# Kernel tuning notes

Measured on AMD Instinct MI355X. Metric: run time of the kernel, lower is better.

The kernel has to match this reference:

```python
import jax, jax.numpy as jnp
import numpy as np

DIM = 512
HEADS = 8
DH = DIM // HEADS          # 64, dim_head = dim // 8
M = DIM // 2               # 256 landmarks
ITERS = 6                  # pinv iterations
KS = 33                    # residual depthwise conv kernel (lucidrains default)
N_LAYERS = 2
LN_EPS = 1e-5


def layer_norm(x, scale, bias):
    mu = x.mean(-1, keepdims=True)
    var = ((x - mu) ** 2).mean(-1, keepdims=True)
    return (x - mu) * jax.lax.rsqrt(var + LN_EPS) * scale + bias


def sinusoidal_pe(T, d, dtype):
    pos = np.arange(T)[:, None]
    div = np.exp(np.arange(0, d, 2) * (-np.log(10000.0) / d))
    pe = np.zeros((T, d), dtype=np.float32)
    pe[:, 0::2] = np.sin(pos * div)
    pe[:, 1::2] = np.cos(pos * div)
    return jnp.asarray(pe, dtype=dtype)


def iter_pinv(x):
    # Newton-Schulz Moore-Penrose iteration (lucidrains), global-max scaling
    ax = jnp.abs(x)
    denom = ax.sum(-1).max() * ax.sum(-2).max()
    z = jnp.swapaxes(x, -1, -2) / denom
    I = jnp.eye(x.shape[-1], dtype=x.dtype)
    for _ in range(ITERS):
        xz = x @ z
        z = 0.25 * (z @ (13.0 * I - xz @ (15.0 * I - xz @ (7.0 * I - xz))))
    return z


def nystrom_attention(x, qkv_w, out_w, out_b, conv_w):
    b, n, d = x.shape
    pad = (-n) % M                       # left-pad so seq divisible by M
    xp = jnp.pad(x, ((0, 0), (pad, 0), (0, 0)))
    N = n + pad
    q, k, v = [t.reshape(b, N, HEADS, DH).transpose(0, 2, 1, 3)
               for t in jnp.split(xp @ qkv_w, 3, axis=-1)]  # each [b,h,N,dh]
    q = q * (DH ** -0.5)
    l = N // M                           # segment length per landmark
    q_l = q.reshape(b, HEADS, M, l, DH).mean(3)   # [b,h,M,dh]
    k_l = k.reshape(b, HEADS, M, l, DH).mean(3)
    attn1 = jax.nn.softmax(jnp.einsum('bhid,bhjd->bhij', q, k_l), -1)    # [b,h,N,M]
    attn2 = jax.nn.softmax(jnp.einsum('bhid,bhjd->bhij', q_l, k_l), -1)  # [b,h,M,M]
    attn3 = jax.nn.softmax(jnp.einsum('bhid,bhjd->bhij', q_l, k), -1)    # [b,h,M,N]
    out = attn1 @ (iter_pinv(attn2) @ (attn3 @ v))                       # [b,h,N,dh]
    # residual depthwise conv over sequence, per head (groups=heads)
    P = KS // 2
    out = out + jax.lax.conv_general_dilated(
        v, conv_w, (1, 1), ((P, P), (0, 0)),
        dimension_numbers=('NCHW', 'OIHW', 'NCHW'), feature_group_count=HEADS)
    out = out.transpose(0, 2, 1, 3).reshape(b, N, d)
    out = out @ out_w + out_b
    return out[:, -n:]


def setup_inputs() -> dict:
    key = jax.random.key(0)
    ks = jax.random.split(key, 12)
    B, T, IN_DIM = 4, 4095, 1024
    s = 0.02
    return {
        'data': jax.random.normal(ks[0], (B, T, IN_DIM), jnp.float32),
        'fc1_w': jax.random.normal(ks[1], (IN_DIM, DIM), jnp.float32) * s,
        'fc1_b': jnp.zeros((DIM,), jnp.float32),
        'cls_token': jax.random.normal(ks[2], (1, 1, DIM), jnp.float32),
        'ln_scale': jnp.ones((N_LAYERS, DIM), jnp.float32),
        'ln_bias': jnp.zeros((N_LAYERS, DIM), jnp.float32),
        'qkv_w': jax.random.normal(ks[3], (N_LAYERS, DIM, 3 * DIM), jnp.float32) * s,
        'out_w': jax.random.normal(ks[4], (N_LAYERS, DIM, DIM), jnp.float32) * s,
        'out_b': jnp.zeros((N_LAYERS, DIM), jnp.float32),
        'conv_w': jax.random.normal(ks[5], (N_LAYERS, HEADS, 1, KS, 1), jnp.float32) * s,
        'fnorm_scale': jnp.ones((DIM,), jnp.float32),
        'fnorm_bias': jnp.zeros((DIM,), jnp.float32),
        'fcout_w': jax.random.normal(ks[6], (DIM, 1), jnp.float32) * s,
        'fcout_b': jnp.zeros((1,), jnp.float32),
    }


def reference(data, fc1_w, fc1_b, cls_token, ln_scale, ln_bias, qkv_w, out_w,
              out_b, conv_w, fnorm_scale, fnorm_bias, fcout_w, fcout_b):
    B, T, _ = data.shape
    h = jax.nn.relu(data @ fc1_w + fc1_b)
    h = h + sinusoidal_pe(T, DIM, h.dtype)
    cls = jnp.broadcast_to(cls_token, (B, 1, DIM))
    h = jnp.concatenate([cls, h], axis=1)
    for i in range(N_LAYERS):
        h = h + nystrom_attention(layer_norm(h, ln_scale[i], ln_bias[i]),
                                  qkv_w[i], out_w[i], out_b[i], conv_w[i])
    h = layer_norm(h, fnorm_scale, fnorm_bias)
    logits = (h[:, 0] @ fcout_w + fcout_b)[:, 0]
    y_prob = jax.nn.sigmoid(logits)
    y_hat = (y_prob > 0.5).astype(jnp.int32)
    return logits, y_prob, y_hat
```

## Files before the change

### kernel.cpp

```cpp
#include <hip/hip_runtime.h>
#include <math.h>

typedef long long ll;
typedef __attribute__((ext_vector_type(8))) short short8;
typedef __attribute__((ext_vector_type(4))) float f32x4;

#define NBATCH 4
#define TSEQ   4095
#define NTOK   4096
#define DMODEL 512
#define NHEAD  8
#define DHEAD  64
#define NLAND  256
#define INDIM  1024
#define KCONV  33
#define NBH    32
#define NSPLIT 8

__device__ __forceinline__ float bred(float* red, float v, int tid, int op){
  red[tid] = v; __syncthreads();
  for (int s = 128; s > 0; s >>= 1){
    if (tid < s) red[tid] = op ? fmaxf(red[tid], red[tid+s]) : (red[tid] + red[tid+s]);
    __syncthreads();
  }
  float r = red[0];
  __syncthreads();
  return r;
}

__device__ __forceinline__ short f2bf(float f){
  unsigned u = __float_as_uint(f);
  u += 0x7fff + ((u>>16)&1);
  return (short)(u>>16);
}
__device__ __forceinline__ float bf2f(short s){
  return __uint_as_float(((unsigned)(unsigned short)s) << 16);
}

__global__ __launch_bounds__(256) void pe_table_k(float* __restrict__ pe){
  int idx = blockIdx.x*256 + threadIdx.x;
  if (idx >= TSEQ*DMODEL) return;
  int c = idx & 511; int t = idx >> 9;
  const double NEG = -9.210340371976184 / 512.0;
  double div = exp((double)(c & ~1) * NEG);
  double ang = (double)t * div;
  pe[idx] = (c & 1) ? (float)cos(ang) : (float)sin(ang);
}

__global__ __launch_bounds__(256) void pe_cls_add_k(float* __restrict__ hb, const float* __restrict__ cls,
                                                    const float* __restrict__ pe){
  ll idx = (ll)blockIdx.x*256 + threadIdx.x;
  int c = (int)(idx & 511);
  ll rn = idx >> 9;
  int n = (int)(rn & 4095);
  if (n == 0) hb[idx] = cls[c];
  else        hb[idx] += pe[(ll)(n-1)*512 + c];
}

__global__ __launch_bounds__(256) void ln_rows_k(const float* __restrict__ in, short* __restrict__ out,
                                                 const float* __restrict__ sc, const float* __restrict__ bi){
  __shared__ float red[256];
  ll row = blockIdx.x;
  const float* xr = in + row*DMODEL;
  short* orow = out + row*DMODEL;
  int tid = threadIdx.x;
  float v0 = xr[tid], v1 = xr[tid+256];
  float mu = bred(red, v0+v1, tid, 0) * (1.f/512.f);
  float d0 = v0-mu, d1 = v1-mu;
  float var = bred(red, d0*d0 + d1*d1, tid, 0) * (1.f/512.f);
  float inv = 1.f / sqrtf(var + 1e-5f);
  orow[tid]     = f2bf(d0*inv*sc[tid]     + bi[tid]);
  orow[tid+256] = f2bf(d1*inv*sc[tid+256] + bi[tid+256]);
}

template<int BM, int BN, int AB, int BB, int CB, int SW>
__global__ __launch_bounds__(256)
void mgemm(const void* __restrict__ Av, const void* __restrict__ Bv,
           void* __restrict__ Cv, const void* __restrict__ Ev,
           const float* __restrict__ bias,
           int Mr, int K, int lda, int ldb, int ldc,
           ll sA, ll sB, ll sC,
           float c0, float c1, int flags)
{
  constexpr int MI = BM/32, NJ = BN/32;
  __shared__ __align__(16) short As[BM*64];
  __shared__ __align__(16) short Bs[BN*64];
  int z = blockIdx.z;
  int bx = blockIdx.x, by = blockIdx.y;
  if (SW){
    int nwg = gridDim.x*gridDim.y;
    int lin = by*gridDim.x + bx;
    int q = nwg >> 3, r = nwg & 7;
    int xcd = lin & 7, idx = lin >> 3;
    int wg = (xcd < r) ? (xcd*(q+1) + idx) : (r*(q+1) + (xcd - r)*q + idx);
    bx = wg % gridDim.x; by = wg / gridDim.x;
  }
  int n0 = bx*BN, m0 = by*BM;
  int tid = threadIdx.x;
  int lane = tid & 63, w = tid >> 6;
  int wr = w >> 1, wc = w & 1;
  int l15 = lane & 15, l4 = lane >> 4;

  f32x4 acc[MI][NJ];
  #pragma unroll
  for (int i = 0; i < MI; i++)
    #pragma unroll
    for (int j = 0; j < NJ; j++) acc[i][j] = (f32x4){0.f,0.f,0.f,0.f};

  for (int k0 = 0; k0 < K; k0 += 64){
    #pragma unroll
    for (int it = 0; it < BM/32; ++it){
      int tau = tid + 256*it;
      int row = tau >> 3, slot = tau & 7;
      int grow = m0 + row;
      short8 v;
      if (AB){
        if (grow < Mr) v = *(const short8*)((const short*)Av + (ll)z*sA + (ll)grow*lda + k0 + slot*8);
        else v = (short8){0,0,0,0,0,0,0,0};
      } else {
        f32x4 p0 = {0.f,0.f,0.f,0.f}, p1 = {0.f,0.f,0.f,0.f};
        if (grow < Mr){
          const float* ap = (const float*)Av + (ll)z*sA + (ll)grow*lda + k0 + slot*8;
          p0 = *(const f32x4*)ap; p1 = *(const f32x4*)(ap+4);
        }
        v[0]=f2bf(p0[0]); v[1]=f2bf(p0[1]); v[2]=f2bf(p0[2]); v[3]=f2bf(p0[3]);
        v[4]=f2bf(p1[0]); v[5]=f2bf(p1[1]); v[6]=f2bf(p1[2]); v[7]=f2bf(p1[3]);
      }
      ((short8*)As)[row*8 + (slot ^ (row&7))] = v;
    }
    #pragma unroll
    for (int it = 0; it < BN/32; ++it){
      int tau = tid + 256*it;
      int n = tau & (BN-1), slot = tau >> (BN==128 ? 7 : 6);
      short8 v;
      if (BB){
        const short* bp = (const short*)Bv + (ll)z*sB + (ll)(k0 + slot*8)*ldb + n0 + n;
        #pragma unroll
        for (int i = 0; i < 8; i++) v[i] = bp[(ll)i*ldb];
      } else {
        const float* bp = (const float*)Bv + (ll)z*sB + (ll)(k0 + slot*8)*ldb + n0 + n;
        #pragma unroll
        for (int i = 0; i < 8; i++) v[i] = f2bf(bp[(ll)i*ldb]);
      }
      ((short8*)Bs)[n*8 + (slot ^ (n&7))] = v;
    }
    __syncthreads();
    #pragma unroll
    for (int kc = 0; kc < 2; kc++){
      short8 af[MI], bfr[NJ];
      #pragma unroll
      for (int i = 0; i < MI; i++){
        int row = wr*(BM/2) + i*16 + l15;
        int g = kc*4 + l4;
        af[i] = ((short8*)As)[row*8 + (g ^ (row&7))];
      }
      #pragma unroll
      for (int j = 0; j < NJ; j++){
        int col = wc*(BN/2) + j*16 + l15;
        int g = kc*4 + l4;
        bfr[j] = ((short8*)Bs)[col*8 + (g ^ (col&7))];
      }
      #pragma unroll
      for (int i = 0; i < MI; i++)
        #pragma unroll
        for (int j = 0; j < NJ; j++)
          acc[i][j] = __builtin_amdgcn_mfma_f32_16x16x32_bf16(af[i], bfr[j], acc[i][j], 0, 0, 0);
    }
    __syncthreads();
  }

  #pragma unroll
  for (int i = 0; i < MI; i++){
    int rbase = m0 + wr*(BM/2) + i*16 + l4*4;
    #pragma unroll
    for (int j = 0; j < NJ; j++){
      int col = n0 + wc*(BN/2) + j*16 + l15;
      #pragma unroll
      for (int r = 0; r < 4; r++){
        int m = rbase + r;
        if (m >= Mr) continue;
        float v = acc[i][j][r];
        if (flags & 4){
          float ev = CB ? bf2f(((const short*)Ev + (ll)z*sC)[(ll)m*ldc + col])
                        : ((const float*)Ev + (ll)z*sC)[(ll)m*ldc + col];
          v = c0 * ev + c1 * v;
        }
        if (flags & 1) v += bias[col];
        if (flags & 2) v = fmaxf(v, 0.f);
        int om = (flags & 16) ? (m + m/TSEQ + 1) : m;
        ll ci = (ll)z*sC + (ll)om*ldc + col;
        if (CB){
          short* Cs = (short*)Cv;
          if (flags & 8) v += bf2f(Cs[ci]);
          Cs[ci] = f2bf(v);
        } else {
          float* Cf = (float*)Cv;
          if (flags & 8) v += Cf[ci];
          Cf[ci] = v;
        }
      }
    }
  }
}

__global__ __launch_bounds__(256)
void gemm_nt(const short* __restrict__ A, const short* __restrict__ Bm, float* __restrict__ C,
             int lda, int ldb, int ldc,
             ll sAb, ll sAh, ll sBb, ll sBh, ll sCb, ll sCh,
             float alpha)
{
  __shared__ float As[64][65];
  __shared__ float Bs[64][65];
  int z = blockIdx.z; int b = z >> 3; int h = z & 7;
  A  += (ll)b*sAb + (ll)h*sAh;
  Bm += (ll)b*sBb + (ll)h*sBh;
  C  += (ll)b*sCb + (ll)h*sCh;
  int n0 = blockIdx.x*64, m0 = blockIdx.y*64;
  int tid = threadIdx.x;
  int kk = tid & 63, rr = tid >> 6;
  #pragma unroll
  for (int r = 0; r < 16; r++){
    As[rr + 4*r][kk] = bf2f(A [(ll)(m0 + rr + 4*r)*lda + kk]);
    Bs[rr + 4*r][kk] = bf2f(Bm[(ll)(n0 + rr + 4*r)*ldb + kk]);
  }
  __syncthreads();
  int tx = tid & 15, ty = tid >> 4;
  float acc[4][4] = {};
  for (int k = 0; k < 64; k++){
    float a[4], bv[4];
    #pragma unroll
    for (int i = 0; i < 4; i++) a[i] = As[ty + 16*i][k];
    #pragma unroll
    for (int j = 0; j < 4; j++) bv[j] = Bs[tx + 16*j][k];
    #pragma unroll
    for (int i = 0; i < 4; i++)
      #pragma unroll
      for (int j = 0; j < 4; j++)
        acc[i][j] += a[i]*bv[j];
  }
  #pragma unroll
  for (int i = 0; i < 4; i++)
    #pragma unroll
    for (int j = 0; j < 4; j++)
      C[(ll)(m0 + ty + 16*i)*ldc + n0 + tx + 16*j] = alpha * acc[i][j];
}

__global__ __launch_bounds__(256)
void mflash_k(const short* __restrict__ Q, const short* __restrict__ K,
              const short* __restrict__ V, short* __restrict__ O,
              int ldq, int ldk, int ldv, int ldo, int nkeys, float alpha,
              ll sQb, ll sQh, ll sKb, ll sKh, ll sVb, ll sVh, ll sOb, ll sOh)
{
  __shared__ __align__(16) short Qs[64*64];
  __shared__ __align__(16) short Ks[64*64];
  __shared__ __align__(16) short Vs[64*64];
  __shared__ __align__(16) short Ps[64*64];
  __shared__ float Sl[64][68];
  __shared__ float m_l[64], s_l[64], scl[64];
  int z = blockIdx.z; int b = z >> 3; int h = z & 7;
  Q += (ll)b*sQb + (ll)h*sQh;
  K += (ll)b*sKb + (ll)h*sKh;
  V += (ll)b*sVb + (ll)h*sVh;
  O += (ll)b*sOb + (ll)h*sOh;
  int m0 = blockIdx.x*64;
  int tid = threadIdx.x;
  int lane = tid & 63, w = tid >> 6;
  int l15 = lane & 15, l4 = lane >> 4;
  int wr = w >> 1, wc = w & 1;

  #pragma unroll
  for (int it = 0; it < 2; it++){
    int tau = tid + 256*it;
    int row = tau >> 3, slot = tau & 7;
    short8 v = *(const short8*)(Q + (ll)(m0 + row)*ldq + slot*8);
    ((short8*)Qs)[row*8 + (slot ^ (row&7))] = v;
  }
  if (tid < 64){ m_l[tid] = -1e30f; s_l[tid] = 0.f; }
  f32x4 o[2][2];
  #pragma unroll
  for (int i = 0; i < 2; i++)
    #pragma unroll
    for (int j = 0; j < 2; j++) o[i][j] = (f32x4){0.f,0.f,0.f,0.f};

  for (int n0 = 0; n0 < nkeys; n0 += 64){
    __syncthreads();
    #pragma unroll
    for (int it = 0; it < 2; it++){
      int tau = tid + 256*it;
      int row = tau >> 3, slot = tau & 7;
      short8 v = *(const short8*)(K + (ll)(n0 + row)*ldk + slot*8);
      ((short8*)Ks)[row*8 + (slot ^ (row&7))] = v;
    }
    #pragma unroll
    for (int it = 0; it < 2; it++){
      int key = (tid >> 3) + 32*it;
      int d0 = (tid & 7)*8;
      short8 v = *(const short8*)(V + (ll)(n0 + key)*ldv + d0);
      #pragma unroll
      for (int j = 0; j < 8; j++){
        int d = d0 + j;
        Vs[d*64 + (((key>>3) ^ (d&7))<<3) + (key&7)] = v[j];
      }
    }
    __syncthreads();
    f32x4 s[2][2];
    #pragma unroll
    for (int i = 0; i < 2; i++)
      #pragma unroll
      for (int j = 0; j < 2; j++) s[i][j] = (f32x4){0.f,0.f,0.f,0.f};
    #pragma unroll
    for (int kc = 0; kc < 2; kc++){
      short8 aq[2], bk[2];
      int g = kc*4 + l4;
      #pragma unroll
      for (int i = 0; i < 2; i++){
        int row = wr*32 + i*16 + l15;
        aq[i] = ((short8*)Qs)[row*8 + (g ^ (row&7))];
      }
      #pragma unroll
      for (int j = 0; j < 2; j++){
        int key = wc*32 + j*16 + l15;
        bk[j] = ((short8*)Ks)[key*8 + (g ^ (key&7))];
      }
      #pragma unroll
      for (int i = 0; i < 2; i++)
        #pragma unroll
        for (int j = 0; j < 2; j++)
          s[i][j] = __builtin_amdgcn_mfma_f32_16x16x32_bf16(aq[i], bk[j], s[i][j], 0, 0, 0);
    }
    #pragma unroll
    for (int i = 0; i < 2; i++)
      #pragma unroll
      for (int j = 0; j < 2; j++)
        #pragma unroll
        for (int r = 0; r < 4; r++)
          Sl[wr*32 + i*16 + l4*4 + r][wc*32 + j*16 + l15] = s[i][j][r] * alpha;
    __syncthreads();
    {
      int row = tid >> 2, q = tid & 3, cb = q*16;
      float sv[16];
      float cmax = -1e30f;
      #pragma unroll
      for (int cc = 0; cc < 16; cc++){ sv[cc] = Sl[row][cb+cc]; cmax = fmaxf(cmax, sv[cc]); }
      cmax = fmaxf(cmax, __shfl_xor(cmax, 1));
      cmax = fmaxf(cmax, __shfl_xor(cmax, 2));
      float mprev = m_l[row];
      float newm = fmaxf(mprev, cmax);
      float lsum = 0.f;
      short8 pv0, pv1;
      #pragma unroll
      for (int cc = 0; cc < 8; cc++){ float e = expf(sv[cc]-newm); lsum += e; pv0[cc] = f2bf(e); }
      #pragma unroll
      for (int cc = 0; cc < 8; cc++){ float e = expf(sv[8+cc]-newm); lsum += e; pv1[cc] = f2bf(e); }
      lsum += __shfl_xor(lsum, 1);
      lsum += __shfl_xor(lsum, 2);
      ((short8*)Ps)[row*8 + ((2*q)   ^ (row&7))] = pv0;
      ((short8*)Ps)[row*8 + ((2*q+1) ^ (row&7))] = pv1;
      if (q == 0){
        float scale = expf(mprev - newm);
        m_l[row] = newm;
        s_l[row] = s_l[row]*scale + lsum;
        scl[row] = scale;
      }
    }
    __syncthreads();
    #pragma unroll
    for (int i = 0; i < 2; i++)
      #pragma unroll
      for (int r = 0; r < 4; r++){
        float sc = scl[wr*32 + i*16 + l4*4 + r];
        #pragma unroll
        for (int j = 0; j < 2; j++) o[i][j][r] *= sc;
      }
    #pragma unroll
    for (int kc = 0; kc < 2; kc++){
      short8 ap[2], bv[2];
      int g = kc*4 + l4;
      #pragma unroll
      for (int i = 0; i < 2; i++){
        int row = wr*32 + i*16 + l15;
        ap[i] = ((short8*)Ps)[row*8 + (g ^ (row&7))];
      }
      #pragma unroll
      for (int j = 0; j < 2; j++){
        int d = wc*32 + j*16 + l15;
        bv[j] = ((short8*)Vs)[d*8 + (g ^ (d&7))];
      }
      #pragma unroll
      for (int i = 0; i < 2; i++)
        #pragma unroll
        for (int j = 0; j < 2; j++)
          o[i][j] = __builtin_amdgcn_mfma_f32_16x16x32_bf16(ap[i], bv[j], o[i][j], 0, 0, 0);
    }
  }
  #pragma unroll
  for (int i = 0; i < 2; i++)
    #pragma unroll
    for (int j = 0; j < 2; j++)
      #pragma unroll
      for (int r = 0; r < 4; r++){
        int row = wr*32 + i*16 + l4*4 + r;
        int col = wc*32 + j*16 + l15;
        O[(ll)(m0 + row)*ldo + col] = f2bf(o[i][j][r] / s_l[row]);
      }
}

__global__ __launch_bounds__(256)
void mflash3_part_k(const short* __restrict__ Q, const short* __restrict__ K,
                    const short* __restrict__ V,
                    float* __restrict__ po, float* __restrict__ pm, float* __restrict__ pl,
                    int ldq, int ldk, int ldv,
                    ll sQb, ll sQh, ll sKb, ll sKh, ll sVb, ll sVh)
{
  __shared__ __align__(16) short Qs[64*64];
  __shared__ __align__(16) short Ks[64*64];
  __shared__ __align__(16) short Vs[64*64];
  __shared__ __align__(16) short Ps[64*64];
  __shared__ float Sl[64][68];
  __shared__ float m_l[64], s_l[64], scl[64];
  int z = blockIdx.z; int b = z >> 3; int h = z & 7;
  int split = blockIdx.y;
  Q += (ll)b*sQb + (ll)h*sQh;
  K += (ll)b*sKb + (ll)h*sKh;
  V += (ll)b*sVb + (ll)h*sVh;
  int m0 = blockIdx.x*64;
  int koff = split * (NTOK/NSPLIT);
  int tid = threadIdx.x;
  int lane = tid & 63, w = tid >> 6;
  int l15 = lane & 15, l4 = lane >> 4;
  int wr = w >> 1, wc = w & 1;

  #pragma unroll
  for (int it = 0; it < 2; it++){
    int tau = tid + 256*it;
    int row = tau >> 3, slot = tau & 7;
    short8 v = *(const short8*)(Q + (ll)(m0 + row)*ldq + slot*8);
    ((short8*)Qs)[row*8 + (slot ^ (row&7))] = v;
  }
  if (tid < 64){ m_l[tid] = -1e30f; s_l[tid] = 0.f; }
  f32x4 o[2][2];
  #pragma unroll
  for (int i = 0; i < 2; i++)
    #pragma unroll
    for (int j = 0; j < 2; j++) o[i][j] = (f32x4){0.f,0.f,0.f,0.f};

  for (int n0 = koff; n0 < koff + NTOK/NSPLIT; n0 += 64){
    __syncthreads();
    #pragma unroll
    for (int it = 0; it < 2; it++){
      int tau = tid + 256*it;
      int row = tau >> 3, slot = tau & 7;
      short8 v = *(const short8*)(K + (ll)(n0 + row)*ldk + slot*8);
      ((short8*)Ks)[row*8 + (slot ^ (row&7))] = v;
    }
    #pragma unroll
    for (int it = 0; it < 2; it++){
      int key = (tid >> 3) + 32*it;
      int d0 = (tid & 7)*8;
      short8 v = *(const short8*)(V + (ll)(n0 + key)*ldv + d0);
      #pragma unroll
      for (int j = 0; j < 8; j++){
        int d = d0 + j;
        Vs[d*64 + (((key>>3) ^ (d&7))<<3) + (key&7)] = v[j];
      }
    }
    __syncthreads();
    f32x4 s[2][2];
    #pragma unroll
    for (int i = 0; i < 2; i++)
      #pragma unroll
      for (int j = 0; j < 2; j++) s[i][j] = (f32x4){0.f,0.f,0.f,0.f};
    #pragma unroll
    for (int kc = 0; kc < 2; kc++){
      short8 aq[2], bk[2];
      int g = kc*4 + l4;
      #pragma unroll
      for (int i = 0; i < 2; i++){
        int row = wr*32 + i*16 + l15;
        aq[i] = ((short8*)Qs)[row*8 + (g ^ (row&7))];
      }
      #pragma unroll
      for (int j = 0; j < 2; j++){
        int key = wc*32 + j*16 + l15;
        bk[j] = ((short8*)Ks)[key*8 + (g ^ (key&7))];
      }
      #pragma unroll
      for (int i = 0; i < 2; i++)
        #pragma unroll
        for (int j = 0; j < 2; j++)
          s[i][j] = __builtin_amdgcn_mfma_f32_16x16x32_bf16(aq[i], bk[j], s[i][j], 0, 0, 0);
    }
    #pragma unroll
    for (int i = 0; i < 2; i++)
      #pragma unroll
      for (int j = 0; j < 2; j++)
        #pragma unroll
        for (int r = 0; r < 4; r++)
          Sl[wr*32 + i*16 + l4*4 + r][wc*32 + j*16 + l15] = s[i][j][r];
    __syncthreads();
    {
      int row = tid >> 2, q = tid & 3, cb = q*16;
      float sv[16];
      float cmax = -1e30f;
      #pragma unroll
      for (int cc = 0; cc < 16; cc++){ sv[cc] = Sl[row][cb+cc]; cmax = fmaxf(cmax, sv[cc]); }
      cmax = fmaxf(cmax, __shfl_xor(cmax, 1));
      cmax = fmaxf(cmax, __shfl_xor(cmax, 2));
      float mprev = m_l[row];
      float newm = fmaxf(mprev, cmax);
      float lsum = 0.f;
      short8 pv0, pv1;
      #pragma unroll
      for (int cc = 0; cc < 8; cc++){ float e = expf(sv[cc]-newm); lsum += e; pv0[cc] = f2bf(e); }
      #pragma unroll
      for (int cc = 0; cc < 8; cc++){ float e = expf(sv[8+cc]-newm); lsum += e; pv1[cc] = f2bf(e); }
      lsum += __shfl_xor(lsum, 1);
      lsum += __shfl_xor(lsum, 2);
      ((short8*)Ps)[row*8 + ((2*q)   ^ (row&7))] = pv0;
      ((short8*)Ps)[row*8 + ((2*q+1) ^ (row&7))] = pv1;
      if (q == 0){
        float scale = expf(mprev - newm);
        m_l[row] = newm;
        s_l[row] = s_l[row]*scale + lsum;
        scl[row] = scale;
      }
    }
    __syncthreads();
    #pragma unroll
    for (int i = 0; i < 2; i++)
      #pragma unroll
      for (int r = 0; r < 4; r++){
        float sc = scl[wr*32 + i*16 + l4*4 + r];
        #pragma unroll
        for (int j = 0; j < 2; j++) o[i][j][r] *= sc;
      }
    #pragma unroll
    for (int kc = 0; kc < 2; kc++){
      short8 ap[2], bv[2];
      int g = kc*4 + l4;
      #pragma unroll
      for (int i = 0; i < 2; i++){
        int row = wr*32 + i*16 + l15;
        ap[i] = ((short8*)Ps)[row*8 + (g ^ (row&7))];
      }
      #pragma unroll
      for (int j = 0; j < 2; j++){
        int d = wc*32 + j*16 + l15;
        bv[j] = ((short8*)Vs)[d*8 + (g ^ (d&7))];
      }
      #pragma unroll
      for (int i = 0; i < 2; i++)
        #pragma unroll
        for (int j = 0; j < 2; j++)
          o[i][j] = __builtin_amdgcn_mfma_f32_16x16x32_bf16(ap[i], bv[j], o[i][j], 0, 0, 0);
    }
  }
  int bs = z*NSPLIT + split;
  #pragma unroll
  for (int i = 0; i < 2; i++)
    #pragma unroll
    for (int j = 0; j < 2; j++)
      #pragma unroll
      for (int r = 0; r < 4; r++){
        int row = wr*32 + i*16 + l4*4 + r;
        int col = wc*32 + j*16 + l15;
        po[((ll)bs*NLAND + m0 + row)*64 + col] = o[i][j][r];
      }
  if (tid < 64){
    pm[(ll)bs*NLAND + m0 + tid] = m_l[tid];
    pl[(ll)bs*NLAND + m0 + tid] = s_l[tid];
  }
}

__global__ __launch_bounds__(256)
void flash3_comb_k(const float* __restrict__ po, const float* __restrict__ pm,
                   const float* __restrict__ pl, short* __restrict__ av){
  int bh = blockIdx.y;
  int row = blockIdx.x*4 + (threadIdx.x >> 6);
  int col = threadIdx.x & 63;
  float ms = -1e30f;
  float mv[NSPLIT];
  #pragma unroll
  for (int s = 0; s < NSPLIT; s++){
    mv[s] = pm[((ll)bh*NSPLIT + s)*NLAND + row];
    ms = fmaxf(ms, mv[s]);
  }
  float osum = 0.f, lsum = 0.f;
  #pragma unroll
  for (int s = 0; s < NSPLIT; s++){
    float wgt = expf(mv[s] - ms);
    osum += wgt * po[(((ll)bh*NSPLIT + s)*NLAND + row)*64 + col];
    lsum += wgt * pl[((ll)bh*NSPLIT + s)*NLAND + row];
  }
  av[((ll)bh*NLAND + row)*64 + col] = f2bf(osum / lsum);
}

__global__ __launch_bounds__(256) void softmax_rows_k(float* __restrict__ data, short* __restrict__ out16,
                                                      int cols){
  __shared__ float red[256];
  float* row = data + (ll)blockIdx.x * cols;
  short* row16 = out16 ? out16 + (ll)blockIdx.x * cols : nullptr;
  int tid = threadIdx.x;
  float m = -1e30f;
  for (int c = tid; c < cols; c += 256) m = fmaxf(m, row[c]);
  m = bred(red, m, tid, 1);
  float s = 0.f;
  for (int c = tid; c < cols; c += 256){ float e = expf(row[c] - m); row[c] = e; s += e; }
  s = bred(red, s, tid, 0);
  float inv = 1.f/s;
  for (int c = tid; c < cols; c += 256){
    float p = row[c] * inv;
    row[c] = p;
    if (row16) row16[c] = f2bf(p);
  }
}

__global__ __launch_bounds__(256) void landmarks_k(const short* __restrict__ qkv,
                                                   short* __restrict__ ql, short* __restrict__ kl){
  int idx = blockIdx.x*256 + threadIdx.x;
  int d = idx & 63;
  int i = (idx >> 6) & 255;
  int h = (idx >> 14) & 7;
  int b = idx >> 17;
  const short* base = qkv + ((ll)b*NTOK + (ll)i*16)*1536 + h*64 + d;
  float sq = 0.f, sk = 0.f;
  #pragma unroll
  for (int l = 0; l < 16; l++){ sq += bf2f(base[l*1536]); sk += bf2f(base[l*1536 + 512]); }
  ql[idx] = f2bf(sq * (0.125f/16.f));
  kl[idx] = f2bf(sk * (1.f/16.f));
}

__global__ void init_scal_k(unsigned* s){ s[0] = 0u; s[1] = 0u; }

__global__ __launch_bounds__(256) void a2_maxsums_k(const float* __restrict__ a2, unsigned* __restrict__ gm){
  __shared__ float red[256];
  const float* A = a2 + (ll)blockIdx.x*65536;
  int tid = threadIdx.x;
  float cs = 0.f, rs = 0.f;
  for (int i = 0; i < 256; i++) cs += A[i*256 + tid];
  for (int j = 0; j < 256; j++) rs += A[tid*256 + j];
  float cmax = bred(red, cs, tid, 1);
  float rmax = bred(red, rs, tid, 1);
  if (tid == 0){
    atomicMax(gm + 0, __float_as_uint(rmax));
    atomicMax(gm + 1, __float_as_uint(cmax));
  }
}

__global__ __launch_bounds__(256) void zinit_k(const float* __restrict__ a2, short* __restrict__ z,
                                               const unsigned* __restrict__ gm){
  float inv = 1.f / (__uint_as_float(gm[0]) * __uint_as_float(gm[1]));
  int idx = blockIdx.x*256 + threadIdx.x;
  int j = idx & 255, i = (idx >> 8) & 255, bh = idx >> 16;
  z[idx] = f2bf(a2[(ll)bh*65536 + j*256 + i] * inv);
}

__global__ __launch_bounds__(256) void dwconv_add_k(const short* __restrict__ qkv,
                                                    const float* __restrict__ cw, short* __restrict__ out){
  __shared__ float sv[160][64];
  __shared__ float w[KCONV];
  int z = blockIdx.y; int b = z >> 3; int h = z & 7;
  int t0 = blockIdx.x * 128;
  int tid = threadIdx.x;
  if (tid < KCONV) w[tid] = cw[h*KCONV + tid];
  const short* vbase = qkv + (ll)b*NTOK*1536 + 1024 + h*64;
  for (int e = tid; e < 160*64; e += 256){
    int r = e >> 6, d = e & 63;
    int t = t0 - 16 + r;
    sv[r][d] = (t >= 0 && t < NTOK) ? bf2f(vbase[(ll)t*1536 + d]) : 0.f;
  }
  __syncthreads();
  short* obase = out + (ll)b*NTOK*512 + h*64;
  for (int e = tid; e < 128*64; e += 256){
    int r = e >> 6, d = e & 63;
    float s = 0.f;
    #pragma unroll
    for (int kk = 0; kk < KCONV; kk++) s += sv[r+kk][d]*w[kk];
    ll oi = (ll)(t0+r)*512 + d;
    obase[oi] = f2bf(bf2f(obase[oi]) + s);
  }
}

__global__ __launch_bounds__(256) void head_k(const float* __restrict__ hb, const float* __restrict__ fns,
      const float* __restrict__ fnb, const float* __restrict__ fw, const float* __restrict__ fb,
      float* __restrict__ out){
  __shared__ float red[256];
  int b = blockIdx.x;
  const float* xr = hb + (ll)b*NTOK*DMODEL;
  int tid = threadIdx.x;
  float v0 = xr[tid], v1 = xr[tid+256];
  float mu = bred(red, v0+v1, tid, 0) * (1.f/512.f);
  float d0 = v0-mu, d1 = v1-mu;
  float var = bred(red, d0*d0 + d1*d1, tid, 0) * (1.f/512.f);
  float inv = 1.f/sqrtf(var + 1e-5f);
  float y0 = d0*inv*fns[tid]     + fnb[tid];
  float y1 = d1*inv*fns[tid+256] + fnb[tid+256];
  float dot = bred(red, y0*fw[tid] + y1*fw[tid+256], tid, 0);
  if (tid == 0){
    float logit = dot + fb[0];
    float prob = 1.f/(1.f + expf(-logit));
    out[b] = logit; out[4+b] = prob; out[8+b] = (prob > 0.5f) ? 1.f : 0.f;
  }
}

extern "C" void kernel_launch(void* const* d_in, const int* in_sizes, int n_in,
                              void* d_out, int out_size, void* d_ws, size_t ws_size,
                              hipStream_t stream)
{
  (void)in_sizes; (void)n_in; (void)out_size;
  const float* data  = (const float*)d_in[0];
  const float* fc1_w = (const float*)d_in[1];
  const float* fc1_b = (const float*)d_in[2];
  const float* cls   = (const float*)d_in[3];
  const float* ln_s  = (const float*)d_in[4];
  const float* ln_b  = (const float*)d_in[5];
  const float* qkv_w = (const float*)d_in[6];
  const float* out_w = (const float*)d_in[7];
  const float* out_b = (const float*)d_in[8];
  const float* convw = (const float*)d_in[9];
  const float* fns   = (const float*)d_in[10];
  const float* fnb   = (const float*)d_in[11];
  const float* fcw   = (const float*)d_in[12];
  const float* fcb   = (const float*)d_in[13];
  float* out = (float*)d_out;
  float* ws  = (float*)d_ws;

  float* h    = ws;
  short* xb   = (short*)(h + 8388608);
  short* qkvh = xb + 8388608;
  short* ql   = qkvh + 25165824;
  short* kl   = ql + 524288;
  float* a2f  = (float*)(kl + 524288);
  short* a2h  = (short*)(a2f + 2097152);
  short* zA   = a2h + 2097152;
  short* zB   = zA + 2097152;
  short* t1   = zB + 2097152;
  short* t2   = t1 + 2097152;
  short* t3   = t2 + 2097152;
  short* av   = t3 + 2097152;
  short* y2   = av + 524288;
  float* po   = (float*)(y2 + 524288);
  float* pm   = po + 4194304;
  float* pl   = pm + 65536;
  float* pe   = pl + 65536;
  unsigned* scal = (unsigned*)(pe + 2097152);

  const size_t NEED = (size_t)((char*)(scal + 2) - (char*)ws);
  if (ws_size < NEED) return;

  pe_table_k<<<(TSEQ*DMODEL + 255)/256, 256, 0, stream>>>(pe);
  mgemm<128,128,0,0,0,1><<<dim3(4, 128, 1), 256, 0, stream>>>(
      data, fc1_w, h, nullptr, fc1_b,
      NBATCH*TSEQ, INDIM, INDIM, DMODEL, DMODEL,
      0, 0, 0, 0.f, 0.f, 1|2|16);
  pe_cls_add_k<<<(NBATCH*NTOK*DMODEL)/256, 256, 0, stream>>>(h, cls, pe);

  for (int L = 0; L < 2; L++){
    const float* qw = qkv_w + (ll)L*DMODEL*1536;
    const float* ow = out_w + (ll)L*DMODEL*DMODEL;
    const float* ob = out_b + (ll)L*DMODEL;
    const float* cw = convw + (ll)L*NHEAD*KCONV;

    ln_rows_k<<<NBATCH*NTOK, 256, 0, stream>>>(h, xb, ln_s + L*DMODEL, ln_b + L*DMODEL);
    mgemm<128,128,1,0,1,1><<<dim3(12, 128, 1), 256, 0, stream>>>(
        xb, qw, qkvh, nullptr, nullptr,
        NBATCH*NTOK, DMODEL, DMODEL, 1536, 1536,
        0, 0, 0, 0.f, 0.f, 0);
    landmarks_k<<<2048, 256, 0, stream>>>(qkvh, ql, kl);

    gemm_nt<<<dim3(4, 4, NBH), 256, 0, stream>>>(
        ql, kl, a2f, 64, 64, 256,
        131072, 16384, 131072, 16384, 524288, 65536, 1.f);
    softmax_rows_k<<<NBH*NLAND, 256, 0, stream>>>(a2f, a2h, 256);

    init_scal_k<<<1, 1, 0, stream>>>(scal);
    a2_maxsums_k<<<NBH, 256, 0, stream>>>(a2f, scal);
    zinit_k<<<8192, 256, 0, stream>>>(a2f, zA, scal);

    short* zc = zA; short* zn = zB;
    for (int it = 0; it < 6; it++){
      mgemm<64,64,1,1,1,0><<<dim3(4, 4, NBH), 256, 0, stream>>>(
          a2h, zc, t1, nullptr, nullptr, 256, 256, 256, 256, 256,
          65536, 65536, 65536, 0.f, 0.f, 0);
      mgemm<64,64,1,1,1,0><<<dim3(4, 4, NBH), 256, 0, stream>>>(
          t1, t1, t2, t1, nullptr, 256, 256, 256, 256, 256,
          65536, 65536, 65536, 7.f, -1.f, 4);
      mgemm<64,64,1,1,1,0><<<dim3(4, 4, NBH), 256, 0, stream>>>(
          t1, t2, t3, t1, nullptr, 256, 256, 256, 256, 256,
          65536, 65536, 65536, 15.f, -1.f, 4);
      mgemm<64,64,1,1,1,0><<<dim3(4, 4, NBH), 256, 0, stream>>>(
          zc, t3, zn, zc, nullptr, 256, 256, 256, 256, 256,
          65536, 65536, 65536, 3.25f, -0.25f, 4);
      short* tmp = zc; zc = zn; zn = tmp;
    }

    mflash3_part_k<<<dim3(4, NSPLIT, NBH), 256, 0, stream>>>(
        ql, qkvh + 512, qkvh + 1024, po, pm, pl,
        64, 1536, 1536,
        131072, 16384, (ll)NTOK*1536, 64, (ll)NTOK*1536, 64);
    flash3_comb_k<<<dim3(64, NBH), 256, 0, stream>>>(po, pm, pl, av);

    mgemm<64,64,1,1,1,0><<<dim3(1, 4, NBH), 256, 0, stream>>>(
        zc, av, y2, nullptr, nullptr, 256, 256, 256, 64, 64,
        65536, 16384, 16384, 0.f, 0.f, 0);

    mflash_k<<<dim3(64, 1, NBH), 256, 0, stream>>>(
        qkvh, kl, y2, xb,
        1536, 64, 64, 512, NLAND, 0.125f,
        (ll)NTOK*1536, 64, 131072, 16384, 131072, 16384, (ll)NTOK*512, 64);

    dwconv_add_k<<<dim3(32, NBH), 256, 0, stream>>>(qkvh, cw, xb);

    mgemm<128,128,1,0,0,1><<<dim3(4, 128, 1), 256, 0, stream>>>(
        xb, ow, h, nullptr, ob,
        NBATCH*NTOK, DMODEL, DMODEL, DMODEL, DMODEL,
        0, 0, 0, 0.f, 0.f, 1|8);
  }

  head_k<<<4, 256, 0, stream>>>(h, fns, fnb, fcw, fcb, out);
}
```

Before: 1.300 ms.

## Pre-convert inputs and weights to bf16 with transposed weight layout for GEMMs

Adds kernels that convert the input data to bf16 and transpose the fc1, qkv and out weight matrices into an N-major bf16 layout. A new B-load mode lets the big GEMMs read B with contiguous 16-byte vector loads instead of eight strided scalar fp32 loads with in-loop conversion. The positional-encoding table now uses float sin/cos instead of double precision. This costs extra workspace and a few extra launches plus one pass over the input data, and the float trig may change PE values slightly at large positions.

Result: no change. 1.308 ms (+0.6%).

```diff
diff --git a/kernel.cpp b/kernel.cpp
--- a/kernel.cpp
+++ b/kernel.cpp
@@ -43,8 +43,8 @@
   int c = idx & 511; int t = idx >> 9;
   const double NEG = -9.210340371976184 / 512.0;
   double div = exp((double)(c & ~1) * NEG);
-  double ang = (double)t * div;
-  pe[idx] = (c & 1) ? (float)cos(ang) : (float)sin(ang);
+  float ang = (float)((double)t * div);
+  pe[idx] = (c & 1) ? cosf(ang) : sinf(ang);
 }
 
 __global__ __launch_bounds__(256) void pe_cls_add_k(float* __restrict__ hb, const float* __restrict__ cls,
@@ -57,6 +57,37 @@
   else        hb[idx] += pe[(ll)(n-1)*512 + c];
 }
 
+__global__ __launch_bounds__(256) void cvt_bf16_k(const float* __restrict__ in, short* __restrict__ out, int n8){
+  int idx = blockIdx.x*256 + threadIdx.x;
+  for (int i = idx; i < n8; i += gridDim.x*256){
+    const f32x4* p = (const f32x4*)(in + (ll)i*8);
+    f32x4 a = p[0], b = p[1];
+    short8 v;
+    v[0]=f2bf(a[0]); v[1]=f2bf(a[1]); v[2]=f2bf(a[2]); v[3]=f2bf(a[3]);
+    v[4]=f2bf(b[0]); v[5]=f2bf(b[1]); v[6]=f2bf(b[2]); v[7]=f2bf(b[3]);
+    ((short8*)out)[i] = v;
+  }
+}
+
+__global__ __launch_bounds__(256) void transpose_bf16_k(const float* __restrict__ in, short* __restrict__ out,
+                                                        int K, int N, ll sIn, ll sOut){
+  __shared__ float t[64][65];
+  int L = blockIdx.z;
+  in  += (ll)L*sIn;
+  out += (ll)L*sOut;
+  int n0 = blockIdx.x*64, k0 = blockIdx.y*64;
+  int tid = threadIdx.x;
+  for (int e = tid; e < 4096; e += 256){
+    int r = e >> 6, c = e & 63;
+    t[r][c] = in[(ll)(k0 + r)*N + n0 + c];
+  }
+  __syncthreads();
+  for (int e = tid; e < 4096; e += 256){
+    int r = e >> 6, c = e & 63;
+    out[(ll)(n0 + r)*K + k0 + c] = f2bf(t[c][r]);
+  }
+}
+
 __global__ __launch_bounds__(256) void ln_rows_k(const float* __restrict__ in, short* __restrict__ out,
                                                  const float* __restrict__ sc, const float* __restrict__ bi){
   __shared__ float red[256];
@@ -73,7 +104,7 @@
   orow[tid+256] = f2bf(d1*inv*sc[tid+256] + bi[tid+256]);
 }
 
-template<int BM, int BN, int AB, int BB, int CB, int SW>
+template<int BM, int BN, int AB, int BMODE, int CB, int SW>
 __global__ __launch_bounds__(256)
 void mgemm(const void* __restrict__ Av, const void* __restrict__ Bv,
            void* __restrict__ Cv, const void* __restrict__ Ev,
@@ -131,18 +162,24 @@
     #pragma unroll
     for (int it = 0; it < BN/32; ++it){
       int tau = tid + 256*it;
-      int n = tau & (BN-1), slot = tau >> (BN==128 ? 7 : 6);
-      short8 v;
-      if (BB){
-        const short* bp = (const short*)Bv + (ll)z*sB + (ll)(k0 + slot*8)*ldb + n0 + n;
-        #pragma unroll
-        for (int i = 0; i < 8; i++) v[i] = bp[(ll)i*ldb];
+      if (BMODE == 2){
+        int n = tau >> 3, slot = tau & 7;
+        short8 v = *(const short8*)((const short*)Bv + (ll)z*sB + (ll)(n0 + n)*ldb + k0 + slot*8);
+        ((short8*)Bs)[n*8 + (slot ^ (n&7))] = v;
       } else {
-        const float* bp = (const float*)Bv + (ll)z*sB + (ll)(k0 + slot*8)*ldb + n0 + n;
-        #pragma unroll
-        for (int i = 0; i < 8; i++) v[i] = f2bf(bp[(ll)i*ldb]);
-      }
-      ((short8*)Bs)[n*8 + (slot ^ (n&7))] = v;
+        int n = tau & (BN-1), slot = tau >> (BN==128 ? 7 : 6);
+        short8 v;
+        if (BMODE == 1){
+          const short* bp = (const short*)Bv + (ll)z*sB + (ll)(k0 + slot*8)*ldb + n0 + n;
+          #pragma unroll
+          for (int i = 0; i < 8; i++) v[i] = bp[(ll)i*ldb];
+        } else {
+          const float* bp = (const float*)Bv + (ll)z*sB + (ll)(k0 + slot*8)*ldb + n0 + n;
+          #pragma unroll
+          for (int i = 0; i < 8; i++) v[i] = f2bf(bp[(ll)i*ldb]);
+        }
+        ((short8*)Bs)[n*8 + (slot ^ (n&7))] = v;
+      }
     }
     __syncthreads();
     #pragma unroll
@@ -743,28 +780,39 @@
   float* pm   = po + 4194304;
   float* pl   = pm + 65536;
   float* pe   = pl + 65536;
-  unsigned* scal = (unsigned*)(pe + 2097152);
+  short* datab = (short*)(pe + 2097152);
+  short* fc1t  = datab + 16777216;
+  short* qkvt  = fc1t + 524288;
+  short* outt  = qkvt + 1572864;
+  unsigned* scal = (unsigned*)(outt + 524288);
 
   const size_t NEED = (size_t)((char*)(scal + 2) - (char*)ws);
   if (ws_size < NEED) return;
 
   pe_table_k<<<(TSEQ*DMODEL + 255)/256, 256, 0, stream>>>(pe);
-  mgemm<128,128,0,0,0,1><<<dim3(4, 128, 1), 256, 0, stream>>>(
-      data, fc1_w, h, nullptr, fc1_b,
-      NBATCH*TSEQ, INDIM, INDIM, DMODEL, DMODEL,
+  cvt_bf16_k<<<2048, 256, 0, stream>>>(data, datab, (NBATCH*TSEQ*INDIM)/8);
+  transpose_bf16_k<<<dim3(8, 16, 1), 256, 0, stream>>>(fc1_w, fc1t, INDIM, DMODEL, 0, 0);
+  transpose_bf16_k<<<dim3(24, 8, 2), 256, 0, stream>>>(qkv_w, qkvt, DMODEL, 1536,
+                                                       (ll)DMODEL*1536, (ll)1536*DMODEL);
+  transpose_bf16_k<<<dim3(8, 8, 2), 256, 0, stream>>>(out_w, outt, DMODEL, DMODEL,
+                                                      (ll)DMODEL*DMODEL, (ll)DMODEL*DMODEL);
+
+  mgemm<128,128,1,2,0,1><<<dim3(4, 128, 1), 256, 0, stream>>>(
+      datab, fc1t, h, nullptr, fc1_b,
+      NBATCH*TSEQ, INDIM, INDIM, INDIM, DMODEL,
       0, 0, 0, 0.f, 0.f, 1|2|16);
   pe_cls_add_k<<<(NBATCH*NTOK*DMODEL)/256, 256, 0, stream>>>(h, cls, pe);
 
   for (int L = 0; L < 2; L++){
-    const float* qw = qkv_w + (ll)L*DMODEL*1536;
-    const float* ow = out_w + (ll)L*DMODEL*DMODEL;
     const float* ob = out_b + (ll)L*DMODEL;
     const float* cw = convw + (ll)L*NHEAD*KCONV;
+    const short* qwt = qkvt + (ll)L*1536*DMODEL;
+    const short* owt = outt + (ll)L*DMODEL*DMODEL;
 
     ln_rows_k<<<NBATCH*NTOK, 256, 0, stream>>>(h, xb, ln_s + L*DMODEL, ln_b + L*DMODEL);
-    mgemm<128,128,1,0,1,1><<<dim3(12, 128, 1), 256, 0, stream>>>(
-        xb, qw, qkvh, nullptr, nullptr,
-        NBATCH*NTOK, DMODEL, DMODEL, 1536, 1536,
+    mgemm<128,128,1,2,1,1><<<dim3(12, 128, 1), 256, 0, stream>>>(
+        xb, qwt, qkvh, nullptr, nullptr,
+        NBATCH*NTOK, DMODEL, DMODEL, DMODEL, 1536,
         0, 0, 0, 0.f, 0.f, 0);
     landmarks_k<<<2048, 256, 0, stream>>>(qkvh, ql, kl);
 
@@ -811,8 +859,8 @@
 
     dwconv_add_k<<<dim3(32, NBH), 256, 0, stream>>>(qkvh, cw, xb);
 
-    mgemm<128,128,1,0,0,1><<<dim3(4, 128, 1), 256, 0, stream>>>(
-        xb, ow, h, nullptr, ob,
+    mgemm<128,128,1,2,0,1><<<dim3(4, 128, 1), 256, 0, stream>>>(
+        xb, owt, h, nullptr, ob,
         NBATCH*NTOK, DMODEL, DMODEL, DMODEL, DMODEL,
         0, 0, 0, 0.f, 0.f, 1|8);
   }
```
